# Performance work log

Hardware: AMD Instinct MI355X
Metric: run time of the kernel (lower is better)

Reference implementation:

```python
import jax, jax.numpy as jnp
import numpy as np

B, TIN, N, F = 2, 12, 800, 2
H, D = 6, 8
C = H * D          # 48
TP = 10            # prediction steps (= pre_step)
PS5 = TP // 5      # int(pre_step/5) = 2
KW = PS5 + 12      # conv1 kernel width = 14


def setup_inputs() -> dict:
    key = jax.random.key(0)
    it = iter(jax.random.split(key, 40))
    def rn(shape, s=0.1):
        return jax.random.normal(next(it), shape, dtype=jnp.float32) * s
    inp = {}
    inp['x'] = rn((B, TIN, N, F), 1.0)
    inp['T'] = rn((B, TP, N, F - 1), 1.0)
    inp['adj'] = jnp.ones((N, N), dtype=bool)  # softmax(laplace) != 0 is all-True
    for nm in ['Wq_t', 'Wk_t', 'Wv_t', 'Wq_st', 'Wk_st', 'Wv_st']:
        inp[nm] = rn((H, F, D))
    for nm in ['bq_t', 'bk_t', 'bv_t', 'bq_st', 'bk_st', 'bv_st']:
        inp[nm] = rn((H, D))
    inp['conv1_w'] = rn((C, F, 1, KW))
    inp['conv1_b'] = rn((C,))
    inp['Wproj_t'] = rn((C, C)); inp['bproj_t'] = rn((C,))
    inp['Wproj_st'] = rn((C, C)); inp['bproj_st'] = rn((C,))
    for nm in ['xhr_wz', 'xhr_wr', 'xhr_wh']:
        inp[nm] = rn((TIN, 3 * C, C))     # input 2C concat hidden C
    for nm in ['xhr_bz', 'xhr_br', 'xhr_bh']:
        inp[nm] = rn((TIN, N, C))
    for nm in ['last_wz', 'last_wr', 'last_wh']:
        inp[nm] = rn((TP, 2 * C, C))      # input C concat hidden C
    for nm in ['last_bz', 'last_br', 'last_bh']:
        inp[nm] = rn((TP, N, C))
    inp['Wout'] = rn((C, 1)); inp['bout'] = rn((1,))
    return inp


def _gru(xi, h, wz, bz, wr, br, wh, bh):
    xh = jnp.concatenate([xi, h], axis=-1)
    z = jax.nn.sigmoid(xh @ wz + bz)
    r = jax.nn.sigmoid(xh @ wr + br)
    hh = jnp.tanh(jnp.concatenate([xi, r * h], axis=-1) @ wh + bh)
    return (1.0 - z) * h + z * hh


def _forward(adj, x, T, Wq_t, bq_t, Wk_t, bk_t, Wv_t, bv_t,
             Wq_st, bq_st, Wk_st, bk_st, Wv_st, bv_st,
             conv1_w, conv1_b, Wproj_t, bproj_t, Wproj_st, bproj_st,
             xhr_wz, xhr_bz, xhr_wr, xhr_br, xhr_wh, xhr_bh,
             last_wz, last_bz, last_wr, last_br, last_wh, last_bh, Wout, bout):
    scale = 1.0 / np.sqrt(D)
    adjf = adj.astype(jnp.float32)
    # ---- temporal multi-head attention (causal over time, per node) ----
    q = jnp.einsum('btnf,hfd->btnhd', x, Wq_t) + bq_t
    k = jnp.einsum('btnf,hfd->btnhd', x, Wk_t) + bk_t
    v = jnp.einsum('btnf,hfd->btnhd', x, Wv_t) + bv_t
    s = jnp.einsum('btnhd,bsnhd->bnhts', q, k) * scale
    causal = jnp.tril(jnp.ones((TIN, TIN), dtype=bool))
    s = jnp.where(causal, s, -1e9)
    p = jax.nn.softmax(s, axis=-1)
    att_t = jnp.einsum('bnhts,bsnhd->btnhd', p, v).reshape(B, TIN, N, C)
    # ---- spatial multi-head attention (adjacency-weighted, per timestep) ----
    q = jnp.einsum('btnf,hfd->btnhd', x, Wq_st) + bq_st
    k = jnp.einsum('btnf,hfd->btnhd', x, Wk_st) + bk_st
    v = jnp.einsum('btnf,hfd->btnhd', x, Wv_st) + bv_st
    s = jnp.einsum('btnhd,btmhd->bthnm', q, k) * scale
    s = s * adjf  # multiplicative adjacency mask (NOT -inf fill), as in source
    p = jax.nn.softmax(s, axis=-1)
    att_st = jnp.einsum('bthnm,btmhd->btnhd', p, v).reshape(B, TIN, N, C)
    att_stt = jnp.concatenate([att_t @ Wproj_t + bproj_t,
                               att_st @ Wproj_st + bproj_st], axis=-1)  # [B,TIN,N,2C]
    # ---- encoder GRU stack over timesteps 1..TIN-1, cell i has own weights ----
    h0 = jnp.zeros((B, N, C), dtype=x.dtype)
    seq = jnp.swapaxes(att_stt[:, 1:], 0, 1)  # [TIN-1, B, N, 2C]
    def step(h, inp):
        xi, wz, bz, wr, br, wh, bh = inp
        return _gru(xi, h, wz, bz, wr, br, wh, bh), None
    ht, _ = jax.lax.scan(step, h0, (seq, xhr_wz[1:], xhr_bz[1:], xhr_wr[1:],
                                    xhr_br[1:], xhr_wh[1:], xhr_bh[1:]))
    # ---- conv1 over time-extended input ----
    Tcat = jnp.concatenate([jnp.zeros(T.shape[:-1] + (1,), T.dtype), T], axis=-1)
    tpx = jnp.concatenate([x, Tcat], axis=1)                 # [B, TIN+TP, N, F]
    tpx = jnp.concatenate([tpx, tpx[:, :PS5 - 1]], axis=1)   # [B, TIN+TP+PS5-1, N, F]
    lhs = jnp.transpose(tpx, (0, 3, 2, 1))                   # [B, F, N, Ttot]
    conv = jax.lax.conv_general_dilated(lhs, conv1_w, (1, 1), 'VALID',
                                        dimension_numbers=('NCHW', 'OIHW', 'NCHW'))
    pre = jnp.transpose(conv + conv1_b[None, :, None, None], (0, 3, 2, 1))  # [B,TP,N,C]
    # ---- decoder GRU, one cell per step, collecting states ----
    def step2(h, inp):
        xi, wz, bz, wr, br, wh, bh = inp
        h = _gru(xi, h, wz, bz, wr, br, wh, bh)
        return h, h
    _, outs = jax.lax.scan(step2, ht, (jnp.swapaxes(pre, 0, 1), last_wz, last_bz,
                                       last_wr, last_br, last_wh, last_bh))
    out = jnp.swapaxes(outs, 0, 1)  # [B, TP, N, C]
    return out @ Wout + bout        # [B, TP, N, 1]


def reference(x, T, adj, Wq_t, bq_t, Wk_t, bk_t, Wv_t, bv_t,
              Wq_st, bq_st, Wk_st, bk_st, Wv_st, bv_st,
              conv1_w, conv1_b, Wproj_t, bproj_t, Wproj_st, bproj_st,
              xhr_wz, xhr_bz, xhr_wr, xhr_br, xhr_wh, xhr_bh,
              last_wz, last_bz, last_wr, last_br, last_wh, last_bh, Wout, bout):
    return _forward(adj, x, T, Wq_t, bq_t, Wk_t, bk_t, Wv_t, bv_t,
                    Wq_st, bq_st, Wk_st, bk_st, Wv_st, bv_st,
                    conv1_w, conv1_b, Wproj_t, bproj_t, Wproj_st, bproj_st,
                    xhr_wz, xhr_bz, xhr_wr, xhr_br, xhr_wh, xhr_bh,
                    last_wz, last_bz, last_wr, last_br, last_wh, last_bh, Wout, bout)
```

## Files before the change

kernel.cpp:

```cpp
#include <hip/hip_runtime.h>
#include <hip/hip_bf16.h>

typedef __hip_bfloat16 bf16;
typedef __attribute__((ext_vector_type(8))) short s8b;
typedef __attribute__((ext_vector_type(4))) float f4;

#define B_ 2
#define TIN_ 12
#define N_ 800
#define F_ 2
#define H_ 6
#define D_ 8
#define C_ 48
#define TP_ 10
#define KW_ 14
#define SCALE 0.35355339059327373f
#define LOG2E 1.4426950408889634f

#define PIN(v) asm volatile("" :: "v"(v))

__device__ __forceinline__ float sigm(float x) { return 1.0f / (1.0f + __expf(-x)); }
__device__ __forceinline__ float tanh_(float x) {
  float e = __expf(-2.0f * x);
  return 2.0f / (1.0f + e) - 1.0f;
}
__device__ __forceinline__ float exp2_(float x) { return __builtin_amdgcn_exp2f(x); }
__device__ __forceinline__ float bfu(unsigned short u) {
  return __uint_as_float((unsigned)u << 16);
}
__device__ __forceinline__ unsigned short f2u(float v) {
  return __bfloat16_as_ushort(__float2bfloat16(v));
}
__device__ __forceinline__ float ldc(const float* p, size_t i) { return p[i]; }
__device__ __forceinline__ float ldc(const bf16* p, size_t i) { return __bfloat162float(p[i]); }
__device__ __forceinline__ void sto(float* p, size_t i, float v) { p[i] = v; }
__device__ __forceinline__ void sto(bf16* p, size_t i, float v) { p[i] = __float2bfloat16(v); }
__device__ __forceinline__ int detect_f32(const void* xv) {
  const unsigned int* xw = (const unsigned int*)xv;
  unsigned int w = xw[threadIdx.x & 63];
  int e = (w >> 7) & 0xFF;
  int bad = ((e >= 1 && e < 96) || (e > 150)) ? 1 : 0;
  unsigned long long m = __ballot(bad);
  return (__popcll(m) >= 16) ? 1 : 0;
}

template <typename TI>
__device__ __forceinline__ void pack_body(
    int gid, const TI* xwz, const TI* xwr, const TI* xwh,
    const TI* lwz, const TI* lwr, const TI* lwh, bf16* pwb) {
  const int total = 21 * 9216;
  if (gid >= total) return;
  int step = gid / 9216, r = gid % 9216;
  int g = r / 3072;  r %= 3072;
  int nt = r / 1024; r %= 1024;
  int c = r / 512;   r %= 512;
  int lane = r / 8, j = r % 8;
  int k = 32 * c + (lane >> 4) * 8 + j;
  int n = nt * 16 + (lane & 15);
  float v = 0.f;
  if (k < 48) {
    if (step < 11) {
      int t = step + 1;
      const TI* w = (g == 0) ? xwz : (g == 1) ? xwr : xwh;
      v = ldc(w, ((size_t)t * 144 + 96 + k) * 48 + n);
    } else {
      int t = step - 11;
      const TI* w = (g == 0) ? lwz : (g == 1) ? lwr : lwh;
      v = ldc(w, ((size_t)t * 96 + 48 + k) * 48 + n);
    }
  }
  pwb[gid] = __float2bfloat16(v);
}

template <typename TI>
__device__ __forceinline__ void temporal_body(
    int gid, const TI* x, const TI* Wq, const TI* Wk, const TI* Wv,
    const TI* bq, const TI* bk, const TI* bv, bf16* att_t) {
  const int total = B_ * (TIN_ - 1) * H_ * N_;
  if (gid >= total) return;
  int n = gid % N_;
  int r = gid / N_;
  int h = r % H_;  r /= H_;
  int t = (r % (TIN_ - 1)) + 1;
  int b = r / (TIN_ - 1);

  float wq[F_][D_], wk[F_][D_], wv[F_][D_], bqv[D_], bkv[D_], bvv[D_];
#pragma unroll
  for (int f = 0; f < F_; ++f)
#pragma unroll
    for (int d = 0; d < D_; ++d) {
      wq[f][d] = ldc(Wq, (h * F_ + f) * D_ + d);
      wk[f][d] = ldc(Wk, (h * F_ + f) * D_ + d);
      wv[f][d] = ldc(Wv, (h * F_ + f) * D_ + d);
    }
#pragma unroll
  for (int d = 0; d < D_; ++d) {
    bqv[d] = ldc(bq, h * D_ + d);
    bkv[d] = ldc(bk, h * D_ + d);
    bvv[d] = ldc(bv, h * D_ + d);
  }
  float xt0 = ldc(x, ((b * TIN_ + t) * N_ + n) * F_ + 0);
  float xt1 = ldc(x, ((b * TIN_ + t) * N_ + n) * F_ + 1);
  float q[D_];
#pragma unroll
  for (int d = 0; d < D_; ++d) q[d] = xt0 * wq[0][d] + xt1 * wq[1][d] + bqv[d];

  float sc[TIN_];
  float mx = -1e30f;
#pragma unroll
  for (int s = 0; s < TIN_; ++s) {
    float xs0 = ldc(x, ((b * TIN_ + s) * N_ + n) * F_ + 0);
    float xs1 = ldc(x, ((b * TIN_ + s) * N_ + n) * F_ + 1);
    float dot = 0.f;
#pragma unroll
    for (int d = 0; d < D_; ++d)
      dot += q[d] * (xs0 * wk[0][d] + xs1 * wk[1][d] + bkv[d]);
    dot *= SCALE;
    sc[s] = (s <= t) ? dot : -1e30f;
    mx = fmaxf(mx, sc[s]);
  }
  float sum = 0.f;
#pragma unroll
  for (int s = 0; s < TIN_; ++s) {
    float p = __expf(sc[s] - mx);
    sc[s] = p;
    sum += p;
  }
  float inv = 1.0f / sum;
  float acc[D_];
#pragma unroll
  for (int d = 0; d < D_; ++d) acc[d] = 0.f;
#pragma unroll
  for (int s = 0; s < TIN_; ++s) {
    float xs0 = ldc(x, ((b * TIN_ + s) * N_ + n) * F_ + 0);
    float xs1 = ldc(x, ((b * TIN_ + s) * N_ + n) * F_ + 1);
#pragma unroll
    for (int d = 0; d < D_; ++d)
      acc[d] += sc[s] * (xs0 * wv[0][d] + xs1 * wv[1][d] + bvv[d]);
  }
  bf16* o = att_t + ((size_t)((b * 11 + (t - 1)) * N_ + n)) * C_ + h * D_;
#pragma unroll
  for (int d = 0; d < D_; ++d) o[d] = __float2bfloat16(acc[d] * inv);
}

template <typename TI>
__device__ __forceinline__ void spatial4_body(
    float2* xs, float (*M)[9], float (*Vw)[3][D_],
    int tile, int ty, int b, int hg,
    const TI* x, const TI* Wq, const TI* Wk, const TI* Wv,
    const TI* bq, const TI* bk, const TI* bv, bf16* att_st) {
  int t = ty + 1;
  int tid = threadIdx.x;

  for (int m = tid; m < N_; m += 832)
    xs[m] = make_float2(ldc(x, ((b * TIN_ + t) * N_ + m) * F_ + 0),
                        ldc(x, ((b * TIN_ + t) * N_ + m) * F_ + 1));
  if (tid < 18) {
    int lh = tid / 9, e = tid % 9, a = e / 3, bb = e % 3;
    int h = hg * 2 + lh;
    float acc = 0.f;
    for (int d = 0; d < 8; ++d) {
      float qa = (a == 0) ? ldc(Wq, (h * 2 + 0) * 8 + d)
               : (a == 1) ? ldc(Wq, (h * 2 + 1) * 8 + d) : ldc(bq, h * 8 + d);
      float kb = (bb == 0) ? ldc(Wk, (h * 2 + 0) * 8 + d)
               : (bb == 1) ? ldc(Wk, (h * 2 + 1) * 8 + d) : ldc(bk, h * 8 + d);
      acc += qa * kb;
    }
    M[lh][e] = acc * SCALE * LOG2E;
  }
  if (tid >= 64 && tid < 64 + 48) {
    int e = tid - 64;
    int lh = e / 24, a = (e % 24) / 8, d = e % 8;
    int h = hg * 2 + lh;
    Vw[lh][a][d] = (a == 0) ? ldc(Wv, (h * 2 + 0) * 8 + d)
                 : (a == 1) ? ldc(Wv, (h * 2 + 1) * 8 + d) : ldc(bv, h * 8 + d);
  }
  __syncthreads();
  if (tid < 800) {
    int row = tid >> 3, ms = tid & 7;
    int n = tile * 100 + row;
    float x0 = xs[n].x, x1 = xs[n].y;
    float A[2], Bc[2], Cc[2];
#pragma unroll
    for (int lh = 0; lh < 2; ++lh) {
      A[lh]  = M[lh][0] * x0 + M[lh][3] * x1 + M[lh][6];
      Bc[lh] = M[lh][1] * x0 + M[lh][4] * x1 + M[lh][7];
      Cc[lh] = M[lh][2] * x0 + M[lh][5] * x1 + M[lh][8];
    }
    float Sp[2] = {0, 0}, S0[2] = {0, 0}, S1[2] = {0, 0};
    for (int m = ms * 100; m < ms * 100 + 100; ++m) {
      float2 xm = xs[m];
#pragma unroll
      for (int lh = 0; lh < 2; ++lh) {
        float p = exp2_(A[lh] * xm.x + Bc[lh] * xm.y + Cc[lh]);
        Sp[lh] += p;
        S0[lh] += p * xm.x;
        S1[lh] += p * xm.y;
      }
    }
#pragma unroll
    for (int lh = 0; lh < 2; ++lh) {
#pragma unroll
      for (int off = 1; off < 8; off <<= 1) {
        Sp[lh] += __shfl_xor(Sp[lh], off);
        S0[lh] += __shfl_xor(S0[lh], off);
        S1[lh] += __shfl_xor(S1[lh], off);
      }
    }
    if (ms == 0) {
      bf16* o = att_st + ((size_t)((b * 11 + ty) * N_ + n)) * C_;
#pragma unroll
      for (int lh = 0; lh < 2; ++lh) {
        int h = hg * 2 + lh;
        float inv = 1.f / Sp[lh];
#pragma unroll
        for (int d = 0; d < 8; ++d)
          o[h * 8 + d] = __float2bfloat16(
              (S0[lh] * Vw[lh][0][d] + S1[lh] * Vw[lh][1][d] + Sp[lh] * Vw[lh][2][d]) * inv);
      }
    }
  }
}

#define SP_BLKS 528
#define TMP_BLKS 127
#define PK_BLKS 233
__global__ __launch_bounds__(832) void k_phase1(
    const void* x,
    const void* Wq_t, const void* Wk_t, const void* Wv_t,
    const void* bq_t, const void* bk_t, const void* bv_t,
    const void* Wq_st, const void* Wk_st, const void* Wv_st,
    const void* bq_st, const void* bk_st, const void* bv_st,
    const void* xwz, const void* xwr, const void* xwh,
    const void* lwz, const void* lwr, const void* lwh,
    bf16* att_t, bf16* att_st, bf16* pwb) {
  __shared__ float2 xs[N_];
  __shared__ float M[2][9];
  __shared__ float Vw[2][3][D_];
  int f32 = detect_f32(x);
  int bx = blockIdx.x;
  if (bx < SP_BLKS) {
    int tile = bx % 8, ty = (bx / 8) % 11, zz = bx / 88;
    int b = zz / 3, hg = zz % 3;
    if (f32)
      spatial4_body<float>(xs, M, Vw, tile, ty, b, hg,
                           (const float*)x, (const float*)Wq_st, (const float*)Wk_st,
                           (const float*)Wv_st, (const float*)bq_st, (const float*)bk_st,
                           (const float*)bv_st, att_st);
    else
      spatial4_body<bf16>(xs, M, Vw, tile, ty, b, hg,
                          (const bf16*)x, (const bf16*)Wq_st, (const bf16*)Wk_st,
                          (const bf16*)Wv_st, (const bf16*)bq_st, (const bf16*)bk_st,
                          (const bf16*)bv_st, att_st);
  } else if (bx < SP_BLKS + TMP_BLKS) {
    int gid = (bx - SP_BLKS) * 832 + threadIdx.x;
    if (f32)
      temporal_body<float>(gid, (const float*)x, (const float*)Wq_t, (const float*)Wk_t,
                           (const float*)Wv_t, (const float*)bq_t, (const float*)bk_t,
                           (const float*)bv_t, att_t);
    else
      temporal_body<bf16>(gid, (const bf16*)x, (const bf16*)Wq_t, (const bf16*)Wk_t,
                          (const bf16*)Wv_t, (const bf16*)bq_t, (const bf16*)bk_t,
                          (const bf16*)bv_t, att_t);
  } else {
    int gid = (bx - SP_BLKS - TMP_BLKS) * 832 + threadIdx.x;
    if (f32)
      pack_body<float>(gid, (const float*)xwz, (const float*)xwr, (const float*)xwh,
                       (const float*)lwz, (const float*)lwr, (const float*)lwh, pwb);
    else
      pack_body<bf16>(gid, (const bf16*)xwz, (const bf16*)xwr, (const bf16*)xwh,
                      (const bf16*)lwz, (const bf16*)lwr, (const bf16*)lwh, pwb);
  }
}

template <typename TI>
__device__ __forceinline__ void projx2_body(
    unsigned short (*rawT)[72], unsigned short (*rawS)[72], unsigned short (*catS)[104],
    int tile, int ty, int b,
    const bf16* att_t, const bf16* att_st,
    const TI* Wpt, const TI* bpt, const TI* Wps, const TI* bps,
    const TI* xwz, const TI* xwr, const TI* xwh,
    const TI* xbz, const TI* xbr, const TI* xbh,
    bf16* xfrag) {
  int t = ty + 1;
  int tid = threadIdx.x;
  int wv = tid >> 6, l = tid & 63;
  int cg = l >> 4, cl = l & 15;

  for (int e = tid; e < 64 * 72; e += 192) {
    int rr = e / 72, c = e % 72;
    int n = tile * 64 + rr; if (n > 799) n = 799;
    size_t base = ((size_t)((b * 11 + ty) * N_ + n)) * C_;
    rawT[rr][c] = (c < 48) ? __bfloat16_as_ushort(att_t[base + c]) : (unsigned short)0;
    rawS[rr][c] = (c < 48) ? __bfloat16_as_ushort(att_st[base + c]) : (unsigned short)0;
  }
  __syncthreads();
#pragma unroll
  for (int q = 0; q < 2; ++q) {
    int nt = 2 * wv + q;
    int half = nt / 3;
    int ncol = (nt - half * 3) * 16 + cl;
    float bias = half ? ldc(bps, ncol) : ldc(bpt, ncol);
    s8b Bf0, Bf1;
#pragma unroll
    for (int j = 0; j < 8; ++j) {
      int k0 = cg * 8 + j;
      int k1 = 32 + cg * 8 + j;
      Bf0[j] = (short)f2u(half ? ldc(Wps, (size_t)k0 * 48 + ncol)
                               : ldc(Wpt, (size_t)k0 * 48 + ncol));
      Bf1[j] = (k1 < 48) ? (short)f2u(half ? ldc(Wps, (size_t)k1 * 48 + ncol)
                                           : ldc(Wpt, (size_t)k1 * 48 + ncol))
                         : (short)0;
    }
    unsigned short (*raw)[72] = half ? rawS : rawT;
#pragma unroll
    for (int mt = 0; mt < 4; ++mt) {
      s8b A0 = *(const s8b*)&raw[mt * 16 + cl][cg * 8];
      s8b A1 = *(const s8b*)&raw[mt * 16 + cl][32 + cg * 8];
      f4 acc = {bias, bias, bias, bias};
      acc = __builtin_amdgcn_mfma_f32_16x16x32_bf16(A0, Bf0, acc, 0, 0, 0);
      acc = __builtin_amdgcn_mfma_f32_16x16x32_bf16(A1, Bf1, acc, 0, 0, 0);
#pragma unroll
      for (int r = 0; r < 4; ++r)
        catS[mt * 16 + cg * 4 + r][nt * 16 + cl] = f2u(acc[r]);
    }
  }
  __syncthreads();
#pragma unroll
  for (int q = 0; q < 3; ++q) {
    int nt = 3 * wv + q;
    int g = nt / 3;
    int jj = (nt - g * 3) * 16 + cl;
    const TI* wx = (g == 0) ? xwz : (g == 1) ? xwr : xwh;
    const TI* bx = (g == 0) ? xbz : (g == 1) ? xbr : xbh;
    s8b Bf[3];
#pragma unroll
    for (int c = 0; c < 3; ++c)
#pragma unroll
      for (int j = 0; j < 8; ++j) {
        int k = c * 32 + cg * 8 + j;
        Bf[c][j] = (short)f2u(ldc(wx, ((size_t)t * 144 + k) * 48 + jj));
      }
#pragma unroll
    for (int mt = 0; mt < 4; ++mt) {
      int nbase = tile * 64 + mt * 16;
      if (nbase >= 800) continue;
      s8b A0 = *(const s8b*)&catS[mt * 16 + cl][cg * 8];
      s8b A1 = *(const s8b*)&catS[mt * 16 + cl][32 + cg * 8];
      s8b A2 = *(const s8b*)&catS[mt * 16 + cl][64 + cg * 8];
      f4 acc;
#pragma unroll
      for (int r = 0; r < 4; ++r)
        acc[r] = ldc(bx, ((size_t)t * N_ + (nbase + cg * 4 + r)) * C_ + jj);
      acc = __builtin_amdgcn_mfma_f32_16x16x32_bf16(A0, Bf[0], acc, 0, 0, 0);
      acc = __builtin_amdgcn_mfma_f32_16x16x32_bf16(A1, Bf[1], acc, 0, 0, 0);
      acc = __builtin_amdgcn_mfma_f32_16x16x32_bf16(A2, Bf[2], acc, 0, 0, 0);
      int grp = b * 50 + tile * 4 + mt;
      size_t idx = ((((size_t)grp * 21 + ty) * 9 + nt) * 64 + l) * 4;
      ushort4 u;
      u.x = f2u(acc[0]); u.y = f2u(acc[1]); u.z = f2u(acc[2]); u.w = f2u(acc[3]);
      *(ushort4*)((unsigned short*)xfrag + idx) = u;
    }
  }
}

template <typename TI>
__device__ __forceinline__ void convx5_body(
    float (*tpw)[KW_][2], float (*cw)[KW_][48], unsigned short (*preS)[72],
    int tile, int t, int b,
    const TI* x, const TI* T,
    const TI* conv1_w, const TI* conv1_b,
    const TI* lwz, const TI* lwr, const TI* lwh,
    const TI* lbz, const TI* lbr, const TI* lbh,
    bf16* xfrag) {
  int tid = threadIdx.x;
  int wv = tid >> 6, l = tid & 63;
  int cg = l >> 4, cl = l & 15;
  int rw = tid / 12, jl = tid % 12;

#pragma unroll 7
  for (int p = 0; p < 7; ++p) {
    int e = tid + p * 192;
    int f = e / (KW_ * 48), rem = e % (KW_ * 48), k = rem / 48, c = rem % 48;
    cw[f][k][c] = ldc(conv1_w, (c * F_ + f) * KW_ + k);
  }
#pragma unroll 10
  for (int p = 0; p < 10; ++p) {
    int e = tid + p * 192;
    if (e < 64 * KW_ * 2) {
      int rr = e / (KW_ * 2), rem = e % (KW_ * 2), k = rem / 2, f = rem % 2;
      int n = tile * 64 + rr; if (n > 799) n = 799;
      int tau = t + k;
      float v;
      if (tau < TIN_) v = ldc(x, ((size_t)(b * TIN_ + tau) * N_ + n) * F_ + f);
      else if (tau < TIN_ + TP_) v = (f == 0) ? 0.f : ldc(T, (size_t)(b * TP_ + (tau - TIN_)) * N_ + n);
      else v = ldc(x, ((size_t)(b * TIN_ + 0) * N_ + n) * F_ + f);
      tpw[rr][k][f] = v;
    }
  }
  for (int e = tid; e < 64 * 24; e += 192)
    preS[e / 24][48 + e % 24] = 0;
  __syncthreads();
  {
    int c0 = jl * 4;
    float acc[4][4];
#pragma unroll
    for (int qq = 0; qq < 4; ++qq)
#pragma unroll
      for (int m = 0; m < 4; ++m) acc[qq][m] = ldc(conv1_b, c0 + m);
#pragma unroll
    for (int f = 0; f < 2; ++f)
      for (int k = 0; k < KW_; ++k) {
        const float4 w4 = *(const float4*)&cw[f][k][c0];
        float wvv[4] = {w4.x, w4.y, w4.z, w4.w};
#pragma unroll
        for (int qq = 0; qq < 4; ++qq) {
          float tv = tpw[rw * 4 + qq][k][f];
#pragma unroll
          for (int m = 0; m < 4; ++m) acc[qq][m] += tv * wvv[m];
        }
      }
#pragma unroll
    for (int qq = 0; qq < 4; ++qq)
#pragma unroll
      for (int m = 0; m < 4; ++m)
        preS[rw * 4 + qq][c0 + m] = f2u(acc[qq][m]);
  }
  __syncthreads();
#pragma unroll
  for (int q = 0; q < 3; ++q) {
    int nt = 3 * wv + q;
    int g = nt / 3;
    int jj = (nt - g * 3) * 16 + cl;
    const TI* wl = (g == 0) ? lwz : (g == 1) ? lwr : lwh;
    const TI* bl = (g == 0) ? lbz : (g == 1) ? lbr : lbh;
    s8b Bf0, Bf1;
#pragma unroll
    for (int j = 0; j < 8; ++j) {
      int k0 = cg * 8 + j;
      int k1 = 32 + cg * 8 + j;
      Bf0[j] = (short)f2u(ldc(wl, ((size_t)t * 96 + k0) * 48 + jj));
      Bf1[j] = (k1 < 48) ? (short)f2u(ldc(wl, ((size_t)t * 96 + k1) * 48 + jj)) : (short)0;
    }
#pragma unroll
    for (int mt = 0; mt < 4; ++mt) {
      int nbase = tile * 64 + mt * 16;
      if (nbase >= 800) continue;
      s8b A0 = *(const s8b*)&preS[mt * 16 + cl][cg * 8];
      s8b A1 = *(const s8b*)&preS[mt * 16 + cl][32 + cg * 8];
      f4 acc;
#pragma unroll
      for (int r = 0; r < 4; ++r)
        acc[r] = ldc(bl, ((size_t)t * N_ + (nbase + cg * 4 + r)) * C_ + jj);
      acc = __builtin_amdgcn_mfma_f32_16x16x32_bf16(A0, Bf0, acc, 0, 0, 0);
      acc = __builtin_amdgcn_mfma_f32_16x16x32_bf16(A1, Bf1, acc, 0, 0, 0);
      int grp = b * 50 + tile * 4 + mt;
      size_t idx = ((((size_t)grp * 21 + (11 + t)) * 9 + nt) * 64 + l) * 4;
      ushort4 u;
      u.x = f2u(acc[0]); u.y = f2u(acc[1]); u.z = f2u(acc[2]); u.w = f2u(acc[3]);
      *(ushort4*)((unsigned short*)xfrag + idx) = u;
    }
  }
}

#define PJ_BLKS 286
#define CV_BLKS 260
__global__ __launch_bounds__(192) void k_xc(
    const bf16* att_t, const bf16* att_st,
    const void* Wpt, const void* bpt, const void* Wps, const void* bps,
    const void* xwz, const void* xwr, const void* xwh,
    const void* xbz, const void* xbr, const void* xbh,
    const void* x, const void* T, const void* cw_, const void* cb,
    const void* lwz, const void* lwr, const void* lwh,
    const void* lbz, const void* lbr, const void* lbh, bf16* xfrag) {
  __shared__ __align__(16) char smem[31744];
  int f32 = detect_f32(x);
  int bx = blockIdx.x;
  if (bx < PJ_BLKS) {
    int tile = bx % 13, ty = (bx / 13) % 11, b = bx / 143;
    auto rawT = (unsigned short(*)[72])smem;
    auto rawS = (unsigned short(*)[72])(smem + 9216);
    auto catS = (unsigned short(*)[104])(smem + 18432);
    if (f32)
      projx2_body<float>(rawT, rawS, catS, tile, ty, b, att_t, att_st,
                         (const float*)Wpt, (const float*)bpt, (const float*)Wps,
                         (const float*)bps, (const float*)xwz, (const float*)xwr,
                         (const float*)xwh, (const float*)xbz, (const float*)xbr,
                         (const float*)xbh, xfrag);
    else
      projx2_body<bf16>(rawT, rawS, catS, tile, ty, b, att_t, att_st,
                        (const bf16*)Wpt, (const bf16*)bpt, (const bf16*)Wps,
                        (const bf16*)bps, (const bf16*)xwz, (const bf16*)xwr,
                        (const bf16*)xwh, (const bf16*)xbz, (const bf16*)xbr,
                        (const bf16*)xbh, xfrag);
  } else {
    int cblk = bx - PJ_BLKS;
    int tile = cblk % 13, t = (cblk / 13) % 10, b = cblk / 130;
    auto tpw  = (float(*)[KW_][2])smem;
    auto cw   = (float(*)[KW_][48])(smem + 7168);
    auto preS = (unsigned short(*)[72])(smem + 12544);
    if (f32)
      convx5_body<float>(tpw, cw, preS, tile, t, b,
                         (const float*)x, (const float*)T, (const float*)cw_, (const float*)cb,
                         (const float*)lwz, (const float*)lwr, (const float*)lwh,
                         (const float*)lbz, (const float*)lbr, (const float*)lbh, xfrag);
    else
      convx5_body<bf16>(tpw, cw, preS, tile, t, b,
                        (const bf16*)x, (const bf16*)T, (const bf16*)cw_, (const bf16*)cb,
                        (const bf16*)lwz, (const bf16*)lwr, (const bf16*)lwh,
                        (const bf16*)lbz, (const bf16*)lbr, (const bf16*)lbh, xfrag);
  }
}

template <bool PF, typename TO>
__device__ __forceinline__ void gru_step12(
    int step, int l, int cg, int cl, int b, int n0,
    s8b (&Wzc)[3][2], s8b (&Wrc)[3][2], s8b (&Whc)[3][2], ushort4 (&cxc)[9],
    s8b (&Wzn)[3][2], s8b (&Wrn)[3][2], s8b (&Whn)[3][2], ushort4 (&cxn)[9],
    const unsigned short* pwb, const unsigned short* xg,
    unsigned short* hT, unsigned short* rhT,
    float (&ho)[3][4], const s8b& WoB0, const s8b& WoB1, float bo, TO* out) {
  s8b hA0 = *(const s8b*)&hT[cl * 72 + cg * 8];
  s8b hA1 = *(const s8b*)&hT[cl * 72 + 32 + cg * 8];
  if (step >= 12) {
    f4 oacc = {bo, bo, bo, bo};
    oacc = __builtin_amdgcn_mfma_f32_16x16x32_bf16(hA0, WoB0, oacc, 0, 0, 0);
    oacc = __builtin_amdgcn_mfma_f32_16x16x32_bf16(hA1, WoB1, oacc, 0, 0, 0);
    if (cl == 0) {
      int t = step - 12;
#pragma unroll
      for (int r = 0; r < 4; ++r)
        sto(out, ((size_t)b * TP_ + t) * N_ + n0 + cg * 4 + r, oacc[r]);
    }
  }
  if (PF) {
    const unsigned short* pb = pwb + (size_t)(step + 1) * 9216 + (size_t)l * 8;
#pragma unroll
    for (int nt = 0; nt < 3; ++nt)
#pragma unroll
      for (int c = 0; c < 2; ++c) {
        Wzn[nt][c] = *(const s8b*)(pb + 0 * 3072 + nt * 1024 + c * 512);
        Wrn[nt][c] = *(const s8b*)(pb + 1 * 3072 + nt * 1024 + c * 512);
        Whn[nt][c] = *(const s8b*)(pb + 2 * 3072 + nt * 1024 + c * 512);
      }
    const unsigned short* xsrc = xg + (size_t)(step + 1) * 2304 + (size_t)l * 4;
#pragma unroll
    for (int gn = 0; gn < 9; ++gn)
      cxn[gn] = *(const ushort4*)(xsrc + gn * 256);
  }
  f4 az[3], ar[3];
#pragma unroll
  for (int nt = 0; nt < 3; ++nt) {
    f4 cz = {bfu(cxc[nt].x), bfu(cxc[nt].y), bfu(cxc[nt].z), bfu(cxc[nt].w)};
    cz = __builtin_amdgcn_mfma_f32_16x16x32_bf16(hA0, Wzc[nt][0], cz, 0, 0, 0);
    cz = __builtin_amdgcn_mfma_f32_16x16x32_bf16(hA1, Wzc[nt][1], cz, 0, 0, 0);
    az[nt] = cz;
    f4 cr = {bfu(cxc[3 + nt].x), bfu(cxc[3 + nt].y), bfu(cxc[3 + nt].z), bfu(cxc[3 + nt].w)};
    cr = __builtin_amdgcn_mfma_f32_16x16x32_bf16(hA0, Wrc[nt][0], cr, 0, 0, 0);
    cr = __builtin_amdgcn_mfma_f32_16x16x32_bf16(hA1, Wrc[nt][1], cr, 0, 0, 0);
    ar[nt] = cr;
  }
  float z[3][4];
#pragma unroll
  for (int nt = 0; nt < 3; ++nt)
#pragma unroll
    for (int r = 0; r < 4; ++r) {
      z[nt][r] = sigm(az[nt][r]);
      float rv = sigm(ar[nt][r]) * ho[nt][r];
      rhT[(cg * 4 + r) * 72 + nt * 16 + cl] = f2u(rv);
    }
  asm volatile("" ::: "memory");
  s8b rA0 = *(const s8b*)&rhT[cl * 72 + cg * 8];
  s8b rA1 = *(const s8b*)&rhT[cl * 72 + 32 + cg * 8];
  f4 ah[3];
#pragma unroll
  for (int nt = 0; nt < 3; ++nt) {
    f4 ch = {bfu(cxc[6 + nt].x), bfu(cxc[6 + nt].y), bfu(cxc[6 + nt].z), bfu(cxc[6 + nt].w)};
    ch = __builtin_amdgcn_mfma_f32_16x16x32_bf16(rA0, Whc[nt][0], ch, 0, 0, 0);
    ch = __builtin_amdgcn_mfma_f32_16x16x32_bf16(rA1, Whc[nt][1], ch, 0, 0, 0);
    ah[nt] = ch;
  }
#pragma unroll
  for (int nt = 0; nt < 3; ++nt)
#pragma unroll
    for (int r = 0; r < 4; ++r) {
      float hn = (1.f - z[nt][r]) * ho[nt][r] + z[nt][r] * tanh_(ah[nt][r]);
      ho[nt][r] = hn;
      hT[(cg * 4 + r) * 72 + nt * 16 + cl] = f2u(hn);
    }
  asm volatile("" ::: "memory");
  if (PF) {
#pragma unroll
    for (int nt = 0; nt < 3; ++nt)
#pragma unroll
      for (int c = 0; c < 2; ++c) {
        PIN(Wzn[nt][c]); PIN(Wrn[nt][c]); PIN(Whn[nt][c]);
      }
#pragma unroll
    for (int gn = 0; gn < 9; ++gn) PIN(cxn[gn]);
  }
}

template <typename TI, typename TO>
__device__ __forceinline__ void gru12_body(
    unsigned short* hT, unsigned short* rhT,
    const unsigned short* xfrag, const unsigned short* pwb,
    const TI* Wout, const TI* bout, TO* out) {
  int l = threadIdx.x;
  int cg = l >> 4, cl = l & 15;
  int blk = blockIdx.x;
  int b = blk / 50;
  int n0 = (blk % 50) * 16;

  for (int e = l; e < 1152; e += 64) { hT[e] = 0; rhT[e] = 0; }
  float bo = ldc(bout, 0);
  s8b WoB0, WoB1;
#pragma unroll
  for (int j = 0; j < 8; ++j) {
    int k0 = cg * 8 + j;
    int k1 = 32 + cg * 8 + j;
    WoB0[j] = (cl == 0) ? (short)f2u(ldc(Wout, k0)) : (short)0;
    WoB1[j] = (cl == 0 && k1 < 48) ? (short)f2u(ldc(Wout, k1)) : (short)0;
  }
  float ho[3][4];
#pragma unroll
  for (int nt = 0; nt < 3; ++nt)
#pragma unroll
    for (int r = 0; r < 4; ++r) ho[nt][r] = 0.f;

  const unsigned short* xg = xfrag + (size_t)blk * 48384;
  s8b WzA[3][2], WrA[3][2], WhA[3][2];
  s8b WzB[3][2], WrB[3][2], WhB[3][2];
  ushort4 cxA[9], cxB[9];
  {
    const unsigned short* pb = pwb + (size_t)l * 8;
#pragma unroll
    for (int nt = 0; nt < 3; ++nt)
#pragma unroll
      for (int c = 0; c < 2; ++c) {
        WzA[nt][c] = *(const s8b*)(pb + 0 * 3072 + nt * 1024 + c * 512);
        WrA[nt][c] = *(const s8b*)(pb + 1 * 3072 + nt * 1024 + c * 512);
        WhA[nt][c] = *(const s8b*)(pb + 2 * 3072 + nt * 1024 + c * 512);
      }
#pragma unroll
    for (int gn = 0; gn < 9; ++gn)
      cxA[gn] = *(const ushort4*)(xg + gn * 256 + l * 4);
  }
  asm volatile("" ::: "memory");

#pragma unroll 1
  for (int s2 = 0; s2 < 10; ++s2) {
    gru_step12<true>(2 * s2, l, cg, cl, b, n0,
                     WzA, WrA, WhA, cxA, WzB, WrB, WhB, cxB,
                     pwb, xg, hT, rhT, ho, WoB0, WoB1, bo, out);
    gru_step12<true>(2 * s2 + 1, l, cg, cl, b, n0,
                     WzB, WrB, WhB, cxB, WzA, WrA, WhA, cxA,
                     pwb, xg, hT, rhT, ho, WoB0, WoB1, bo, out);
  }
  gru_step12<false>(20, l, cg, cl, b, n0,
                    WzA, WrA, WhA, cxA, WzB, WrB, WhB, cxB,
                    pwb, xg, hT, rhT, ho, WoB0, WoB1, bo, out);
  {
    s8b hA0 = *(const s8b*)&hT[cl * 72 + cg * 8];
    s8b hA1 = *(const s8b*)&hT[cl * 72 + 32 + cg * 8];
    f4 oacc = {bo, bo, bo, bo};
    oacc = __builtin_amdgcn_mfma_f32_16x16x32_bf16(hA0, WoB0, oacc, 0, 0, 0);
    oacc = __builtin_amdgcn_mfma_f32_16x16x32_bf16(hA1, WoB1, oacc, 0, 0, 0);
    if (cl == 0) {
#pragma unroll
      for (int r = 0; r < 4; ++r)
        sto(out, ((size_t)b * TP_ + 9) * N_ + n0 + cg * 4 + r, oacc[r]);
    }
  }
}
__global__ __launch_bounds__(64, 1) void k_gru12(
    const void* xin, const bf16* xfrag, const bf16* pwb,
    const void* Wout, const void* bout, void* out) {
  __shared__ alignas(16) unsigned short hT[1152];
  __shared__ alignas(16) unsigned short rhT[1152];
  int f32 = detect_f32(xin);
  if (f32)
    gru12_body<float, float>(hT, rhT,
                             (const unsigned short*)xfrag, (const unsigned short*)pwb,
                             (const float*)Wout, (const float*)bout, (float*)out);
  else
    gru12_body<bf16, bf16>(hT, rhT,
                           (const unsigned short*)xfrag, (const unsigned short*)pwb,
                           (const bf16*)Wout, (const bf16*)bout, (bf16*)out);
}

extern "C" void kernel_launch(void* const* d_in, const int* in_sizes, int n_in,
                              void* d_out, int out_size, void* d_ws, size_t ws_size,
                              hipStream_t stream) {
  (void)in_sizes; (void)n_in; (void)out_size; (void)ws_size;
  const void* x       = d_in[0];
  const void* T       = d_in[1];
  const void* Wq_t    = d_in[3];
  const void* Wk_t    = d_in[4];
  const void* Wv_t    = d_in[5];
  const void* Wq_st   = d_in[6];
  const void* Wk_st   = d_in[7];
  const void* Wv_st   = d_in[8];
  const void* bq_t    = d_in[9];
  const void* bk_t    = d_in[10];
  const void* bv_t    = d_in[11];
  const void* bq_st   = d_in[12];
  const void* bk_st   = d_in[13];
  const void* bv_st   = d_in[14];
  const void* conv1_w = d_in[15];
  const void* conv1_b = d_in[16];
  const void* Wproj_t = d_in[17];
  const void* bproj_t = d_in[18];
  const void* Wproj_st= d_in[19];
  const void* bproj_st= d_in[20];
  const void* xhr_wz  = d_in[21];
  const void* xhr_wr  = d_in[22];
  const void* xhr_wh  = d_in[23];
  const void* xhr_bz  = d_in[24];
  const void* xhr_br  = d_in[25];
  const void* xhr_bh  = d_in[26];
  const void* last_wz = d_in[27];
  const void* last_wr = d_in[28];
  const void* last_wh = d_in[29];
  const void* last_bz = d_in[30];
  const void* last_br = d_in[31];
  const void* last_bh = d_in[32];
  const void* Wout    = d_in[33];
  const void* bout    = d_in[34];

  char* wsb = (char*)d_ws;
  bf16* att_t  = (bf16*)(wsb + 256);
  bf16* att_st = att_t + (size_t)2 * 11 * 800 * 48;
  bf16* xfrag  = att_st + (size_t)2 * 11 * 800 * 48;
  bf16* pwb    = xfrag + (size_t)100 * 21 * 9 * 64 * 4;

  k_phase1<<<SP_BLKS + TMP_BLKS + PK_BLKS, 832, 0, stream>>>(
      x, Wq_t, Wk_t, Wv_t, bq_t, bk_t, bv_t,
      Wq_st, Wk_st, Wv_st, bq_st, bk_st, bv_st,
      xhr_wz, xhr_wr, xhr_wh, last_wz, last_wr, last_wh,
      att_t, att_st, pwb);
  k_xc<<<PJ_BLKS + CV_BLKS, 192, 0, stream>>>(
      att_t, att_st, Wproj_t, bproj_t, Wproj_st, bproj_st,
      xhr_wz, xhr_wr, xhr_wh, xhr_bz, xhr_br, xhr_bh,
      x, T, conv1_w, conv1_b, last_wz, last_wr, last_wh,
      last_bz, last_br, last_bh, xfrag);
  k_gru12<<<100, 64, 0, stream>>>(
      x, xfrag, pwb, Wout, bout, d_out);
}
```

Measured before the change: 117.7 us.

## Prepack projection and GRU input weights into MFMA fragments in phase1

The phase-1 pack kernel now also writes bf16 MFMA B-fragment layouts for the projection weights, the encoder GRU input weights and the decoder GRU input weights. k_xc then reads each fragment with one 16-byte vector load instead of many strided scalar loads and conversions per block. Separately, the spatial attention drops the per-query constant term from the exponent, which softmax normalisation cancels anyway. The cost is more pack blocks in phase 1, plus a larger workspace footprint that must fit the allocation.

Result: faster. 97.73 us (-16.9%).

```diff
diff --git a/kernel.cpp b/kernel.cpp
--- a/kernel.cpp
+++ b/kernel.cpp
@@ -19,6 +19,12 @@
 
 #define PIN(v) asm volatile("" :: "v"(v))
 
+#define PACK_GRU_TOT (21 * 9216)
+#define PACK_PWX_TOT (11 * 9 * 3 * 512)
+#define PACK_PWP_TOT (6 * 2 * 512)
+#define PACK_PWL_TOT (10 * 9 * 2 * 512)
+#define PACK_TOT (PACK_GRU_TOT + PACK_PWX_TOT + PACK_PWP_TOT + PACK_PWL_TOT)
+
 __device__ __forceinline__ float sigm(float x) { return 1.0f / (1.0f + __expf(-x)); }
 __device__ __forceinline__ float tanh_(float x) {
   float e = __expf(-2.0f * x);
@@ -47,26 +53,57 @@
 template <typename TI>
 __device__ __forceinline__ void pack_body(
     int gid, const TI* xwz, const TI* xwr, const TI* xwh,
-    const TI* lwz, const TI* lwr, const TI* lwh, bf16* pwb) {
-  const int total = 21 * 9216;
-  if (gid >= total) return;
-  int step = gid / 9216, r = gid % 9216;
-  int g = r / 3072;  r %= 3072;
-  int nt = r / 1024; r %= 1024;
-  int c = r / 512;   r %= 512;
-  int lane = r / 8, j = r % 8;
-  int k = 32 * c + (lane >> 4) * 8 + j;
-  int n = nt * 16 + (lane & 15);
+    const TI* lwz, const TI* lwr, const TI* lwh,
+    const TI* Wpt, const TI* Wps, bf16* pwb) {
+  if (gid >= PACK_TOT) return;
   float v = 0.f;
-  if (k < 48) {
-    if (step < 11) {
-      int t = step + 1;
+  if (gid < PACK_GRU_TOT) {
+    int step = gid / 9216, r = gid % 9216;
+    int g = r / 3072;  r %= 3072;
+    int nt = r / 1024; r %= 1024;
+    int c = r / 512;   r %= 512;
+    int lane = r / 8, j = r % 8;
+    int k = 32 * c + (lane >> 4) * 8 + j;
+    int n = nt * 16 + (lane & 15);
+    if (k < 48) {
+      if (step < 11) {
+        int t = step + 1;
+        const TI* w = (g == 0) ? xwz : (g == 1) ? xwr : xwh;
+        v = ldc(w, ((size_t)t * 144 + 96 + k) * 48 + n);
+      } else {
+        int t = step - 11;
+        const TI* w = (g == 0) ? lwz : (g == 1) ? lwr : lwh;
+        v = ldc(w, ((size_t)t * 96 + 48 + k) * 48 + n);
+      }
+    }
+  } else {
+    int e2 = gid - PACK_GRU_TOT;
+    if (e2 < PACK_PWX_TOT) {
+      int j = e2 & 7, lane = (e2 >> 3) & 63;
+      int c = (e2 >> 9) % 3, nt = (e2 / 1536) % 9, tt = e2 / 13824;
+      int t = tt + 1;
+      int k = c * 32 + (lane >> 4) * 8 + j;
+      int g = nt / 3, jj = (nt - g * 3) * 16 + (lane & 15);
       const TI* w = (g == 0) ? xwz : (g == 1) ? xwr : xwh;
-      v = ldc(w, ((size_t)t * 144 + 96 + k) * 48 + n);
+      v = ldc(w, ((size_t)t * 144 + k) * 48 + jj);
     } else {
-      int t = step - 11;
-      const TI* w = (g == 0) ? lwz : (g == 1) ? lwr : lwh;
-      v = ldc(w, ((size_t)t * 96 + 48 + k) * 48 + n);
+      int e3 = e2 - PACK_PWX_TOT;
+      if (e3 < PACK_PWP_TOT) {
+        int j = e3 & 7, lane = (e3 >> 3) & 63;
+        int c = (e3 >> 9) & 1, nt = e3 / 1024;
+        int k = c * 32 + (lane >> 4) * 8 + j;
+        int half = nt / 3, ncol = (nt - half * 3) * 16 + (lane & 15);
+        if (k < 48)
+          v = half ? ldc(Wps, (size_t)k * 48 + ncol) : ldc(Wpt, (size_t)k * 48 + ncol);
+      } else {
+        int e4 = e3 - PACK_PWP_TOT;
+        int j = e4 & 7, lane = (e4 >> 3) & 63;
+        int c = (e4 >> 9) & 1, nt = (e4 / 1024) % 9, t = e4 / 9216;
+        int k = c * 32 + (lane >> 4) * 8 + j;
+        int g = nt / 3, jj = (nt - g * 3) * 16 + (lane & 15);
+        const TI* w = (g == 0) ? lwz : (g == 1) ? lwr : lwh;
+        if (k < 48) v = ldc(w, ((size_t)t * 96 + k) * 48 + jj);
+      }
     }
   }
   pwb[gid] = __float2bfloat16(v);
@@ -180,19 +217,18 @@
     int row = tid >> 3, ms = tid & 7;
     int n = tile * 100 + row;
     float x0 = xs[n].x, x1 = xs[n].y;
-    float A[2], Bc[2], Cc[2];
+    float A[2], Bc[2];
 #pragma unroll
     for (int lh = 0; lh < 2; ++lh) {
       A[lh]  = M[lh][0] * x0 + M[lh][3] * x1 + M[lh][6];
       Bc[lh] = M[lh][1] * x0 + M[lh][4] * x1 + M[lh][7];
-      Cc[lh] = M[lh][2] * x0 + M[lh][5] * x1 + M[lh][8];
     }
     float Sp[2] = {0, 0}, S0[2] = {0, 0}, S1[2] = {0, 0};
     for (int m = ms * 100; m < ms * 100 + 100; ++m) {
       float2 xm = xs[m];
 #pragma unroll
       for (int lh = 0; lh < 2; ++lh) {
-        float p = exp2_(A[lh] * xm.x + Bc[lh] * xm.y + Cc[lh]);
+        float p = exp2_(A[lh] * xm.x + Bc[lh] * xm.y);
         Sp[lh] += p;
         S0[lh] += p * xm.x;
         S1[lh] += p * xm.y;
@@ -224,7 +260,7 @@
 
 #define SP_BLKS 528
 #define TMP_BLKS 127
-#define PK_BLKS 233
+#define PK_BLKS 534
 __global__ __launch_bounds__(832) void k_phase1(
     const void* x,
     const void* Wq_t, const void* Wk_t, const void* Wv_t,
@@ -233,6 +269,7 @@
     const void* bq_st, const void* bk_st, const void* bv_st,
     const void* xwz, const void* xwr, const void* xwh,
     const void* lwz, const void* lwr, const void* lwh,
+    const void* Wpt, const void* Wps,
     bf16* att_t, bf16* att_st, bf16* pwb) {
   __shared__ float2 xs[N_];
   __shared__ float M[2][9];
@@ -266,10 +303,12 @@
     int gid = (bx - SP_BLKS - TMP_BLKS) * 832 + threadIdx.x;
     if (f32)
       pack_body<float>(gid, (const float*)xwz, (const float*)xwr, (const float*)xwh,
-                       (const float*)lwz, (const float*)lwr, (const float*)lwh, pwb);
+                       (const float*)lwz, (const float*)lwr, (const float*)lwh,
+                       (const float*)Wpt, (const float*)Wps, pwb);
     else
       pack_body<bf16>(gid, (const bf16*)xwz, (const bf16*)xwr, (const bf16*)xwh,
-                      (const bf16*)lwz, (const bf16*)lwr, (const bf16*)lwh, pwb);
+                      (const bf16*)lwz, (const bf16*)lwr, (const bf16*)lwh,
+                      (const bf16*)Wpt, (const bf16*)Wps, pwb);
   }
 }
 
@@ -278,8 +317,8 @@
     unsigned short (*rawT)[72], unsigned short (*rawS)[72], unsigned short (*catS)[104],
     int tile, int ty, int b,
     const bf16* att_t, const bf16* att_st,
-    const TI* Wpt, const TI* bpt, const TI* Wps, const TI* bps,
-    const TI* xwz, const TI* xwr, const TI* xwh,
+    const unsigned short* pwp, const unsigned short* pwx,
+    const TI* bpt, const TI* bps,
     const TI* xbz, const TI* xbr, const TI* xbh,
     bf16* xfrag) {
   int t = ty + 1;
@@ -301,17 +340,8 @@
     int half = nt / 3;
     int ncol = (nt - half * 3) * 16 + cl;
     float bias = half ? ldc(bps, ncol) : ldc(bpt, ncol);
-    s8b Bf0, Bf1;
-#pragma unroll
-    for (int j = 0; j < 8; ++j) {
-      int k0 = cg * 8 + j;
-      int k1 = 32 + cg * 8 + j;
-      Bf0[j] = (short)f2u(half ? ldc(Wps, (size_t)k0 * 48 + ncol)
-                               : ldc(Wpt, (size_t)k0 * 48 + ncol));
-      Bf1[j] = (k1 < 48) ? (short)f2u(half ? ldc(Wps, (size_t)k1 * 48 + ncol)
-                                           : ldc(Wpt, (size_t)k1 * 48 + ncol))
-                         : (short)0;
-    }
+    s8b Bf0 = *(const s8b*)(pwp + (nt * 2 + 0) * 512 + l * 8);
+    s8b Bf1 = *(const s8b*)(pwp + (nt * 2 + 1) * 512 + l * 8);
     unsigned short (*raw)[72] = half ? rawS : rawT;
 #pragma unroll
     for (int mt = 0; mt < 4; ++mt) {
@@ -331,16 +361,11 @@
     int nt = 3 * wv + q;
     int g = nt / 3;
     int jj = (nt - g * 3) * 16 + cl;
-    const TI* wx = (g == 0) ? xwz : (g == 1) ? xwr : xwh;
     const TI* bx = (g == 0) ? xbz : (g == 1) ? xbr : xbh;
     s8b Bf[3];
 #pragma unroll
     for (int c = 0; c < 3; ++c)
-#pragma unroll
-      for (int j = 0; j < 8; ++j) {
-        int k = c * 32 + cg * 8 + j;
-        Bf[c][j] = (short)f2u(ldc(wx, ((size_t)t * 144 + k) * 48 + jj));
-      }
+      Bf[c] = *(const s8b*)(pwx + (((size_t)ty * 9 + nt) * 3 + c) * 512 + l * 8);
 #pragma unroll
     for (int mt = 0; mt < 4; ++mt) {
       int nbase = tile * 64 + mt * 16;
@@ -370,7 +395,7 @@
     int tile, int t, int b,
     const TI* x, const TI* T,
     const TI* conv1_w, const TI* conv1_b,
-    const TI* lwz, const TI* lwr, const TI* lwh,
+    const unsigned short* pwl,
     const TI* lbz, const TI* lbr, const TI* lbh,
     bf16* xfrag) {
   int tid = threadIdx.x;
@@ -432,16 +457,9 @@
     int nt = 3 * wv + q;
     int g = nt / 3;
     int jj = (nt - g * 3) * 16 + cl;
-    const TI* wl = (g == 0) ? lwz : (g == 1) ? lwr : lwh;
     const TI* bl = (g == 0) ? lbz : (g == 1) ? lbr : lbh;
-    s8b Bf0, Bf1;
-#pragma unroll
-    for (int j = 0; j < 8; ++j) {
-      int k0 = cg * 8 + j;
-      int k1 = 32 + cg * 8 + j;
-      Bf0[j] = (short)f2u(ldc(wl, ((size_t)t * 96 + k0) * 48 + jj));
-      Bf1[j] = (k1 < 48) ? (short)f2u(ldc(wl, ((size_t)t * 96 + k1) * 48 + jj)) : (short)0;
-    }
+    s8b Bf0 = *(const s8b*)(pwl + (((size_t)t * 9 + nt) * 2 + 0) * 512 + l * 8);
+    s8b Bf1 = *(const s8b*)(pwl + (((size_t)t * 9 + nt) * 2 + 1) * 512 + l * 8);
 #pragma unroll
     for (int mt = 0; mt < 4; ++mt) {
       int nbase = tile * 64 + mt * 16;
@@ -467,32 +485,30 @@
 #define CV_BLKS 260
 __global__ __launch_bounds__(192) void k_xc(
     const bf16* att_t, const bf16* att_st,
-    const void* Wpt, const void* bpt, const void* Wps, const void* bps,
-    const void* xwz, const void* xwr, const void* xwh,
+    const void* bpt, const void* bps,
     const void* xbz, const void* xbr, const void* xbh,
     const void* x, const void* T, const void* cw_, const void* cb,
-    const void* lwz, const void* lwr, const void* lwh,
-    const void* lbz, const void* lbr, const void* lbh, bf16* xfrag) {
+    const void* lbz, const void* lbr, const void* lbh,
+    const bf16* pwb, bf16* xfrag) {
   __shared__ __align__(16) char smem[31744];
   int f32 = detect_f32(x);
   int bx = blockIdx.x;
+  const unsigned short* pwx = (const unsigned short*)(pwb + PACK_GRU_TOT);
+  const unsigned short* pwp = (const unsigned short*)(pwb + PACK_GRU_TOT + PACK_PWX_TOT);
+  const unsigned short* pwl = (const unsigned short*)(pwb + PACK_GRU_TOT + PACK_PWX_TOT + PACK_PWP_TOT);
   if (bx < PJ_BLKS) {
     int tile = bx % 13, ty = (bx / 13) % 11, b = bx / 143;
     auto rawT = (unsigned short(*)[72])smem;
     auto rawS = (unsigned short(*)[72])(smem + 9216);
     auto catS = (unsigned short(*)[104])(smem + 18432);
     if (f32)
-      projx2_body<float>(rawT, rawS, catS, tile, ty, b, att_t, att_st,
-                         (const float*)Wpt, (const float*)bpt, (const float*)Wps,
-                         (const float*)bps, (const float*)xwz, (const float*)xwr,
-                         (const float*)xwh, (const float*)xbz, (const float*)xbr,
-                         (const float*)xbh, xfrag);
+      projx2_body<float>(rawT, rawS, catS, tile, ty, b, att_t, att_st, pwp, pwx,
+                         (const float*)bpt, (const float*)bps,
+                         (const float*)xbz, (const float*)xbr, (const float*)xbh, xfrag);
     else
-      projx2_body<bf16>(rawT, rawS, catS, tile, ty, b, att_t, att_st,
-                        (const bf16*)Wpt, (const bf16*)bpt, (const bf16*)Wps,
-                        (const bf16*)bps, (const bf16*)xwz, (const bf16*)xwr,
-                        (const bf16*)xwh, (const bf16*)xbz, (const bf16*)xbr,
-                        (const bf16*)xbh, xfrag);
+      projx2_body<bf16>(rawT, rawS, catS, tile, ty, b, att_t, att_st, pwp, pwx,
+                        (const bf16*)bpt, (const bf16*)bps,
+                        (const bf16*)xbz, (const bf16*)xbr, (const bf16*)xbh, xfrag);
   } else {
     int cblk = bx - PJ_BLKS;
     int tile = cblk % 13, t = (cblk / 13) % 10, b = cblk / 130;
@@ -502,13 +518,11 @@
     if (f32)
       convx5_body<float>(tpw, cw, preS, tile, t, b,
                          (const float*)x, (const float*)T, (const float*)cw_, (const float*)cb,
-                         (const float*)lwz, (const float*)lwr, (const float*)lwh,
-                         (const float*)lbz, (const float*)lbr, (const float*)lbh, xfrag);
+                         pwl, (const float*)lbz, (const float*)lbr, (const float*)lbh, xfrag);
     else
       convx5_body<bf16>(tpw, cw, preS, tile, t, b,
                         (const bf16*)x, (const bf16*)T, (const bf16*)cw_, (const bf16*)cb,
-                        (const bf16*)lwz, (const bf16*)lwr, (const bf16*)lwh,
-                        (const bf16*)lbz, (const bf16*)lbr, (const bf16*)lbh, xfrag);
+                        pwl, (const bf16*)lbz, (const bf16*)lbr, (const bf16*)lbh, xfrag);
   }
 }
 
@@ -738,12 +752,13 @@
       x, Wq_t, Wk_t, Wv_t, bq_t, bk_t, bv_t,
       Wq_st, Wk_st, Wv_st, bq_st, bk_st, bv_st,
       xhr_wz, xhr_wr, xhr_wh, last_wz, last_wr, last_wh,
+      Wproj_t, Wproj_st,
       att_t, att_st, pwb);
   k_xc<<<PJ_BLKS + CV_BLKS, 192, 0, stream>>>(
-      att_t, att_st, Wproj_t, bproj_t, Wproj_st, bproj_st,
-      xhr_wz, xhr_wr, xhr_wh, xhr_bz, xhr_br, xhr_bh,
-      x, T, conv1_w, conv1_b, last_wz, last_wr, last_wh,
-      last_bz, last_br, last_bh, xfrag);
+      att_t, att_st, bproj_t, bproj_st,
+      xhr_bz, xhr_br, xhr_bh,
+      x, T, conv1_w, conv1_b, last_bz, last_br, last_bh,
+      pwb, xfrag);
   k_gru12<<<100, 64, 0, stream>>>(
       x, xfrag, pwb, Wout, bout, d_out);
 }
```
